# Kernel tuning notes

Hardware: AMD Instinct MI355X
Metric: run time of the kernel (lower is better)

## Reference

```python
import jax, jax.numpy as jnp
import numpy as np

C = 512
NC = 12
EPS = 1e-5

ADJ = np.array([
    [0,0,0,1,0,1,1,1,1,1,1,1],
    [0,0,0,1,0,1,1,1,1,1,1,1],
    [0,0,0,1,0,1,1,1,1,1,1,1],
    [1,1,1,0,1,1,1,1,1,1,1,1],
    [0,0,0,1,0,1,1,1,1,1,1,1],
    [1,1,1,1,1,0,1,1,1,0,0,0],
    [1,1,1,1,1,1,0,0,0,1,1,1],
    [1,1,1,1,1,1,0,0,0,1,1,1],
    [1,1,1,1,1,1,0,0,0,1,1,1],
    [1,1,1,1,1,0,1,1,1,0,0,0],
    [1,1,1,1,1,0,1,1,1,0,0,0],
    [1,1,1,1,1,0,1,1,1,0,0,0]], dtype=np.float32)
# per-AU region selection: 0=up,1=mid,2=down1,3=down2 (AU1,2,4 up; AU6 mid; AU7 up; AU10 d2; AU12,14,15 d1; AU17,23,24 d2)
SEL = np.array([0,0,0,1,0,3,2,2,2,3,3,3])


def setup_inputs() -> dict:
    key = jax.random.key(0)
    ks = jax.random.split(key, 12)
    B, T = 32, 32
    BT = B * T
    s = (2.0 / C) ** 0.5
    return {
        'x': jax.random.normal(ks[0], (BT, 49, C), jnp.float32),
        'adj_mask': jnp.ones((BT, NC, NC), jnp.float32),
        'region_W': jax.random.normal(ks[1], (4, C, C), jnp.float32) * s,
        'region_b': jnp.zeros((4, C), jnp.float32),
        'region_gamma': jnp.ones((4, C), jnp.float32),
        'region_beta': jnp.zeros((4, C), jnp.float32),
        'upfc_W': jax.random.normal(ks[2], (C, 16), jnp.float32) * 0.02,
        'upfc_b': jnp.zeros((16,), jnp.float32),
        'midfc_W': jax.random.normal(ks[3], (C, 2), jnp.float32) * 0.02,
        'midfc_b': jnp.zeros((2,), jnp.float32),
        'd1fc_W': jax.random.normal(ks[4], (C, 8), jnp.float32) * 0.02,
        'd1fc_b': jnp.zeros((8,), jnp.float32),
        'd2fc_W': jax.random.normal(ks[5], (C, 16), jnp.float32) * 0.02,
        'd2fc_b': jnp.zeros((16,), jnp.float32),
        'class_W': jax.random.normal(ks[6], (NC, C, C), jnp.float32) * s,
        'class_b': jnp.zeros((NC, C), jnp.float32),
        'class_gamma': jnp.ones((NC, C), jnp.float32),
        'class_beta': jnp.zeros((NC, C), jnp.float32),
        'gat_W': jax.random.normal(ks[7], (C, C), jnp.float32) * 0.02,
        'gat_al': jax.random.normal(ks[8], (C,), jnp.float32) * 0.02,
        'gat_ar': jax.random.normal(ks[9], (C,), jnp.float32) * 0.02,
        'tconv_W': jax.random.normal(ks[10], (NC, C, 5), jnp.float32) * 0.1,
        'tconv_b': jnp.zeros((NC, C), jnp.float32),
        'tbn_gamma': jnp.ones((NC,), jnp.float32),
        'tbn_beta': jnp.zeros((NC,), jnp.float32),
        'B': B,
        'T': T,
    }


def _bn(x, gamma, beta, axes):
    # training-mode batch norm: stats over `axes`, affine per remaining channel
    mean = x.mean(axes, keepdims=True)
    var = x.var(axes, keepdims=True)
    return gamma * (x - mean) * jax.lax.rsqrt(var + EPS) + beta


def reference(x, adj_mask, region_W, region_b, region_gamma, region_beta,
              upfc_W, upfc_b, midfc_W, midfc_b, d1fc_W, d1fc_b, d2fc_W, d2fc_b,
              class_W, class_b, class_gamma, class_beta,
              gat_W, gat_al, gat_ar, tconv_W, tconv_b, tbn_gamma, tbn_beta, B, T):
    BT = x.shape[0]
    xg = x.reshape(BT, 7, 7, C)
    x_up = xg[:, :3].reshape(BT, 21, C)
    x_mid = xg[:, 2:5].reshape(BT, 21, C)
    x_down = xg[:, 4:].reshape(BT, 21, C)
    # 4 region LinearBlocks (fc -> BN over (batch,seq) per channel -> relu), batched
    regions = jnp.stack([x_up, x_mid, x_down, x_down])  # [4,BT,21,C]
    h = jnp.einsum('rbsc,rcd->rbsd', regions, region_W) + region_b[:, None, None, :]
    h = jax.nn.relu(_bn(h, region_gamma[:, None, None, :], region_beta[:, None, None, :], (1, 2)))
    up_pred = h[0].mean(1) @ upfc_W + upfc_b
    mid_pred = h[1].mean(1) @ midfc_W + midfc_b
    d1_pred = h[2].mean(1) @ d1fc_W + d1fc_b
    d2_pred = h[3].mean(1) @ d2fc_W + d2fc_b
    # 12 per-AU LinearBlocks, batched over the class dim
    cls_in = h[jnp.asarray(SEL)]  # [12,BT,21,C]
    y = jnp.einsum('nbsc,ncd->nbsd', cls_in, class_W) + class_b[:, None, None, :]
    y = jax.nn.relu(_bn(y, class_gamma[:, None, None, :], class_beta[:, None, None, :], (1, 2)))
    f_v = y.mean(2).transpose(1, 0, 2)  # [BT,12,C]
    # cross-region single-head GAT over the fixed 12-node graph, residual, thred=0.1
    adj = jnp.asarray(ADJ)[None] * adj_mask + jnp.eye(NC, dtype=x.dtype)
    hg = f_v @ gat_W  # [BT,12,C]
    e = jax.nn.leaky_relu((hg @ gat_al)[:, :, None] + (hg @ gat_ar)[:, None, :], 0.2)
    attn = jax.nn.softmax(jnp.where(adj > 0.1, e, -1e9), axis=-1)
    g = jnp.einsum('bij,bjc->bic', attn, hg) + f_v
    # per-class depthwise temporal Conv1d (k=5, pad=2, groups=C), batched over classes
    x4 = g.reshape(B, T, NC, C)
    xp = jnp.pad(x4, ((0, 0), (2, 2), (0, 0), (0, 0)))
    v = sum(xp[:, k:k + T] * tconv_W[None, None, :, :, k] for k in range(5)) + tconv_b[None, None]
    v = v.reshape(BT, NC, C)
    out = jax.nn.relu(_bn(v, tbn_gamma[None, :, None], tbn_beta[None, :, None], (0, 2)))
    return (up_pred, mid_pred, d1_pred, d2_pred, out)
```

## Files before the change

kernel.cpp:

```cpp
#include <hip/hip_runtime.h>
#include <hip/hip_bf16.h>

typedef unsigned short u16;
typedef __attribute__((ext_vector_type(8))) __bf16 bf16x8;
typedef __attribute__((ext_vector_type(8))) u16 u16x8;
typedef __attribute__((ext_vector_type(4))) float floatx4;

#define C_     512
#define NC_    12
#define BT_    1024
#define SEQ_   21
#define M_REG  21504
#define M_GAT  12288

__device__ __forceinline__ float bf2f(u16 u) {
  unsigned int v = ((unsigned int)u) << 16;
  float f; __builtin_memcpy(&f, &v, 4); return f;
}
__device__ __forceinline__ u16 f2bf(float f) {
  unsigned int b; __builtin_memcpy(&b, &f, 4);
  unsigned int r = (b + 0x7FFFu + ((b >> 16) & 1u)) >> 16;
  return (u16)r;
}
__device__ __forceinline__ float ldf(const void* p, size_t i, int f32) {
  return f32 ? ((const float*)p)[i] : bf2f(((const u16*)p)[i]);
}
__device__ __forceinline__ u16 ldbf(const void* p, size_t i, int f32) {
  return f32 ? f2bf(((const float*)p)[i]) : ((const u16*)p)[i];
}
__device__ __forceinline__ void stout(void* p, size_t i, float v, int f32) {
  if (f32) ((float*)p)[i] = v; else ((u16*)p)[i] = f2bf(v);
}

typedef __attribute__((address_space(1))) unsigned int as1_u32;
typedef __attribute__((address_space(3))) unsigned int as3_u32;
__device__ __forceinline__ void gl2lds16(const void* g, void* l) {
  __builtin_amdgcn_global_load_lds((const as1_u32*)g, (as3_u32*)l, 16, 0, 0);
}

__global__ void sent_k(float* __restrict__ o, float val) {
  const int i = blockIdx.x * 256 + threadIdx.x;
  if (i < 16384) o[i] = val;
}

__global__ void detect_k(const u16* __restrict__ x, int* __restrict__ flag) {
  __shared__ int cnt;
  if (threadIdx.x == 0) cnt = 0;
  __syncthreads();
  int bad = 0;
  for (int i = threadIdx.x; i < 4096; i += 256) {
    const float v = bf2f(x[i]);
    const float a = fabsf(v);
    if (!(a <= 1e4f)) bad++;
    else if (a > 0.f && a < 1e-35f) bad++;
  }
  atomicAdd(&cnt, bad);
  __syncthreads();
  if (threadIdx.x == 0) *flag = (cnt > 400) ? 1 : 0;
}

__global__ void zero_stats(float* __restrict__ p, int n) {
  const int id = blockIdx.x * 256 + threadIdx.x;
  if (id < n) p[id] = 0.f;
}

__global__ void transpose512(const void* __restrict__ rW, const void* __restrict__ cW,
                             const void* __restrict__ gW, u16* __restrict__ oR,
                             u16* __restrict__ oC, u16* __restrict__ oG,
                             const int* __restrict__ flagp) {
  const int f32 = *flagp;
  const int z = blockIdx.z;
  const void* src; u16* dst; size_t sofs = 0;
  if (z < 4)       { src = rW; sofs = (size_t)z*262144;     dst = oR + (size_t)z*262144; }
  else if (z < 16) { src = cW; sofs = (size_t)(z-4)*262144; dst = oC + (size_t)(z-4)*262144; }
  else             { src = gW;                              dst = oG; }
  __shared__ u16 t[32][33];
  const int tx = threadIdx.x;
  const int cy = blockIdx.y * 32, dx = blockIdx.x * 32;
  for (int i = threadIdx.y; i < 32; i += 8)
    t[i][tx] = ldbf(src, sofs + (size_t)(cy + i)*512 + dx + tx, f32);
  __syncthreads();
  for (int i = threadIdx.y; i < 32; i += 8)
    dst[(size_t)(dx + i)*512 + cy + tx] = t[tx][i];
}

template<int MODE>
__global__ __launch_bounds__(256)
void gemm_k(const void* __restrict__ Abase, const u16* __restrict__ Wtb,
            const void* __restrict__ biasb, u16* __restrict__ outb,
            float* __restrict__ ssumb, float* __restrict__ ssqb,
            const int* __restrict__ flagp, int pk, int n0)
{
  const int f32 = *flagp;
  const int z = blockIdx.z;
  const int zeff = (MODE == 1) ? (n0 + z) : z;
  const void* A = Abase;
  if (MODE == 1) A = (const void*)((const u16*)Abase +
        (size_t)((pk >> (zeff * 2)) & 3) * ((size_t)M_REG * C_));
  const u16* Wt = Wtb + (size_t)zeff * C_ * C_;
  u16* Out = outb + (size_t)z * (size_t)M_REG * C_;

  __shared__ __align__(16) u16 As[128*32];
  __shared__ __align__(16) u16 Bs[128*32];

  const int tid  = threadIdx.x;
  const int w    = tid >> 6;
  const int lane = tid & 63;
  const int wm   = w >> 1, wn = w & 1;
  const int r16  = lane & 15, q = lane >> 4;

  const int m0  = blockIdx.y * 128;
  const int nn0 = blockIdx.x * 128;

  const int sub = lane >> 2;
  const int kq  = (lane & 3) * 8;
  const int am0 = m0 + w*32 + sub;
  const int am1 = am0 + 16;
  long ga0, ga1;
  if (MODE == 0) {
    const int roff = (pk >> (z * 8)) & 0xFF;
    int q21 = am0 / 21; int rm = am0 - q21*21;
    ga0 = (long)q21*49 + roff + rm;
    q21 = am1 / 21; rm = am1 - q21*21;
    ga1 = (long)q21*49 + roff + rm;
  } else { ga0 = am0; ga1 = am1; }
  const size_t aOff0 = (size_t)ga0 * C_ + kq;
  const size_t aOff1 = (size_t)ga1 * C_ + kq;
  const u16* bSrc0 = Wt + (size_t)(nn0 + w*32 + sub) * C_ + kq;
  const u16* bSrc1 = bSrc0 + (size_t)16 * C_;
  u16* aDstW0 = &As[(w*32 +  0) * 32];
  u16* aDstW1 = &As[(w*32 + 16) * 32];
  u16* bDstW0 = &Bs[(w*32 +  0) * 32];
  u16* bDstW1 = &Bs[(w*32 + 16) * 32];
  u16x8* aLds0 = (u16x8*)&As[(w*32 + sub +  0) * 32 + kq];
  u16x8* aLds1 = (u16x8*)&As[(w*32 + sub + 16) * 32 + kq];

  floatx4 acc[4][4];
  #pragma unroll
  for (int i = 0; i < 4; i++)
    #pragma unroll
    for (int j = 0; j < 4; j++)
      acc[i][j] = (floatx4){0.f, 0.f, 0.f, 0.f};

  for (int kk = 0; kk < C_; kk += 32) {
    if (MODE == 0 && f32) {
      const float* p0 = (const float*)A + aOff0 + kk;
      const float* p1 = (const float*)A + aOff1 + kk;
      const floatx4 f00 = *(const floatx4*)p0;
      const floatx4 f01 = *(const floatx4*)(p0 + 4);
      const floatx4 f10 = *(const floatx4*)p1;
      const floatx4 f11 = *(const floatx4*)(p1 + 4);
      u16x8 va0, va1;
      #pragma unroll
      for (int j = 0; j < 4; j++) {
        va0[j] = f2bf(f00[j]); va0[4+j] = f2bf(f01[j]);
        va1[j] = f2bf(f10[j]); va1[4+j] = f2bf(f11[j]);
      }
      __syncthreads();
      gl2lds16(bSrc0, bDstW0); gl2lds16(bSrc1, bDstW1);
      *aLds0 = va0; *aLds1 = va1;
      __syncthreads();
    } else {
      __syncthreads();
      gl2lds16((const u16*)A + aOff0 + kk, aDstW0);
      gl2lds16((const u16*)A + aOff1 + kk, aDstW1);
      gl2lds16(bSrc0, bDstW0);
      gl2lds16(bSrc1, bDstW1);
      __syncthreads();
    }
    bSrc0 += 32; bSrc1 += 32;
    bf16x8 av[4], bv[4];
    #pragma unroll
    for (int mt = 0; mt < 4; mt++)
      av[mt] = *(const bf16x8*)&As[(wm*64 + mt*16 + r16)*32 + q*8];
    #pragma unroll
    for (int nt = 0; nt < 4; nt++)
      bv[nt] = *(const bf16x8*)&Bs[(wn*64 + nt*16 + r16)*32 + q*8];
    #pragma unroll
    for (int mt = 0; mt < 4; mt++)
      #pragma unroll
      for (int nt = 0; nt < 4; nt++)
        acc[mt][nt] = __builtin_amdgcn_mfma_f32_16x16x32_bf16(av[mt], bv[nt], acc[mt][nt], 0, 0, 0);
  }

  const int colb = nn0 + wn*64;
  const int rowb = m0  + wm*64;
  #pragma unroll
  for (int nt = 0; nt < 4; nt++) {
    const int col = colb + nt*16 + r16;
    float bvv = 0.f;
    if (MODE != 2) bvv = ldf(biasb, (size_t)zeff * C_ + col, f32);
    float s = 0.f, s2 = 0.f;
    #pragma unroll
    for (int mt = 0; mt < 4; mt++) {
      #pragma unroll
      for (int p = 0; p < 4; p++) {
        float v = acc[mt][nt][p] + bvv;
        const int row = rowb + mt*16 + q*4 + p;
        Out[(size_t)row * C_ + col] = f2bf(v);
        s += v; s2 += v*v;
      }
    }
    if (MODE != 2) {
      s  += __shfl_xor(s, 16);  s  += __shfl_xor(s, 32);
      s2 += __shfl_xor(s2, 16); s2 += __shfl_xor(s2, 32);
      if (q == 0) {
        atomicAdd(&ssumb[(size_t)zeff * C_ + col], s);
        atomicAdd(&ssqb [(size_t)zeff * C_ + col], s2);
      }
    }
  }
}

__global__ void bn_region(u16* __restrict__ h, float* __restrict__ hbar,
                          const void* __restrict__ gamma, const void* __restrict__ beta,
                          const float* __restrict__ rsum, const float* __restrict__ rsq,
                          const int* __restrict__ flagp) {
  const int f32 = *flagp;
  const int gid  = blockIdx.x;
  const int r    = gid >> 8;
  const int bt   = ((gid & 255) << 2) + (threadIdx.x >> 6);
  const int lane = threadIdx.x & 63;
  const int d0   = lane * 8;
  const int rd   = r*512 + d0;
  float sc[8], sh[8], accv[8];
  #pragma unroll
  for (int j = 0; j < 8; j++) {
    const float mean = rsum[rd+j] * (1.f/21504.f);
    const float var  = fmaxf(rsq[rd+j] * (1.f/21504.f) - mean*mean, 0.f);
    sc[j] = ldf(gamma, rd+j, f32) * rsqrtf(var + 1e-5f);
    sh[j] = ldf(beta,  rd+j, f32) - mean * sc[j];
    accv[j] = 0.f;
  }
  const size_t base = ((size_t)r * M_REG + (size_t)bt * SEQ_) * C_ + d0;
  #pragma unroll
  for (int s = 0; s < SEQ_; s++) {
    u16x8 vv = *(u16x8*)&h[base + (size_t)s*C_];
    #pragma unroll
    for (int j = 0; j < 8; j++) {
      float v = fmaxf(sc[j] * bf2f(vv[j]) + sh[j], 0.f);
      vv[j] = f2bf(v);
      accv[j] += v;
    }
    *(u16x8*)&h[base + (size_t)s*C_] = vv;
  }
  float* hb = &hbar[((size_t)r * BT_ + bt) * C_ + d0];
  #pragma unroll
  for (int j = 0; j < 8; j++) hb[j] = accv[j] * (1.f/21.f);
}

__global__ void preds_k(const float* __restrict__ hbar,
                        const void* __restrict__ upW,  const void* __restrict__ upB,
                        const void* __restrict__ midW, const void* __restrict__ midB,
                        const void* __restrict__ d1W,  const void* __restrict__ d1B,
                        const void* __restrict__ d2W,  const void* __restrict__ d2B,
                        void* __restrict__ dout, const int* __restrict__ flagp) {
  const int f32 = *flagp;
  const int bt = blockIdx.x;
  __shared__ float hl[4][512];
  for (int i = threadIdx.x; i < 2048; i += 256)
    hl[i >> 9][i & 511] = hbar[((size_t)(i >> 9) * BT_ + bt) * C_ + (i & 511)];
  __syncthreads();
  const int j = threadIdx.x;
  if (j < 42) {
    int r, wdt, col; const void *W, *Bv; size_t oofs;
    if (j < 16)      { r=0; W=upW;  Bv=upB;  wdt=16; col=j;    oofs = (size_t)bt*16 + col; }
    else if (j < 18) { r=1; W=midW; Bv=midB; wdt=2;  col=j-16; oofs = 16384 + (size_t)bt*2 + col; }
    else if (j < 26) { r=2; W=d1W;  Bv=d1B;  wdt=8;  col=j-18; oofs = 18432 + (size_t)bt*8 + col; }
    else             { r=3; W=d2W;  Bv=d2B;  wdt=16; col=j-26; oofs = 26624 + (size_t)bt*16 + col; }
    float acc = ldf(Bv, col, f32);
    for (int d = 0; d < 512; d++) acc += hl[r][d] * ldf(W, d*wdt + col, f32);
    stout(dout, oofs, acc, f32);
  }
}

__global__ void bn_class_mean(const u16* __restrict__ ypre, u16* __restrict__ fv,
                              const void* __restrict__ gamma, const void* __restrict__ beta,
                              const float* __restrict__ csum, const float* __restrict__ csq,
                              const int* __restrict__ flagp, int n0) {
  const int f32 = *flagp;
  const int gid  = blockIdx.x;
  const int zz   = gid >> 8;
  const int bt   = ((gid & 255) << 2) + (threadIdx.x >> 6);
  const int lane = threadIdx.x & 63;
  const int d0   = lane * 8;
  const int n    = n0 + zz;
  const int nd   = n*512 + d0;
  float sc[8], sh[8], accv[8];
  #pragma unroll
  for (int j = 0; j < 8; j++) {
    const float mean = csum[nd+j] * (1.f/21504.f);
    const float var  = fmaxf(csq[nd+j] * (1.f/21504.f) - mean*mean, 0.f);
    sc[j] = ldf(gamma, nd+j, f32) * rsqrtf(var + 1e-5f);
    sh[j] = ldf(beta,  nd+j, f32) - mean * sc[j];
    accv[j] = 0.f;
  }
  const size_t base = ((size_t)zz * M_REG + (size_t)bt * SEQ_) * C_ + d0;
  #pragma unroll
  for (int s = 0; s < SEQ_; s++) {
    const u16x8 vv = *(const u16x8*)&ypre[base + (size_t)s*C_];
    #pragma unroll
    for (int j = 0; j < 8; j++)
      accv[j] += fmaxf(sc[j] * bf2f(vv[j]) + sh[j], 0.f);
  }
  u16x8 ov;
  #pragma unroll
  for (int j = 0; j < 8; j++) ov[j] = f2bf(accv[j] * (1.f/21.f));
  *(u16x8*)&fv[((size_t)bt * NC_ + n) * C_ + d0] = ov;
}

__global__ __launch_bounds__(256)
void gat_k(const u16* __restrict__ hg, const u16* __restrict__ fv,
           const void* __restrict__ al, const void* __restrict__ ar,
           const void* __restrict__ adj_mask, float* __restrict__ g,
           const int* __restrict__ flagp) {
  const int f32 = *flagp;
  const int bt = blockIdx.x;
  __shared__ float hl[12][512];
  __shared__ float alv[12], arv[12], attn[12][12];
  const u16* hgb = hg + (size_t)bt * NC_ * C_;
  for (int i = threadIdx.x; i < 6144; i += 256)
    hl[i >> 9][i & 511] = bf2f(hgb[i]);
  __syncthreads();
  const int w = threadIdx.x >> 6, lane = threadIdx.x & 63;
  for (int i = w; i < 12; i += 4) {
    float pa = 0.f, pr = 0.f;
    #pragma unroll
    for (int jj = 0; jj < 8; jj++) {
      const int c = lane*8 + jj;
      const float hv = hl[i][c];
      pa += hv * ldf(al, c, f32);
      pr += hv * ldf(ar, c, f32);
    }
    #pragma unroll
    for (int off = 32; off; off >>= 1) { pa += __shfl_xor(pa, off); pr += __shfl_xor(pr, off); }
    if (lane == 0) { alv[i] = pa; arv[i] = pr; }
  }
  __syncthreads();
  if (threadIdx.x < 12) {
    const unsigned AM[12] = {0xFE8,0xFE8,0xFE8,0xFF7,0xFE8,0x1DF,
                             0xE3F,0xE3F,0xE3F,0x1DF,0x1DF,0x1DF};
    const int i = threadIdx.x;
    float row[12]; float mx = -1e30f;
    #pragma unroll
    for (int jx = 0; jx < 12; jx++) {
      const float maskv = ldf(adj_mask, (size_t)bt*144 + i*12 + jx, f32);
      const float adjv = (float)((AM[i] >> jx) & 1u) * maskv + (i == jx ? 1.f : 0.f);
      float e;
      if (adjv > 0.1f) {
        const float t = alv[i] + arv[jx];
        e = t > 0.f ? t : 0.2f * t;
      } else e = -1e9f;
      row[jx] = e; mx = fmaxf(mx, e);
    }
    float den = 0.f;
    #pragma unroll
    for (int jx = 0; jx < 12; jx++) { const float ex = __expf(row[jx] - mx); row[jx] = ex; den += ex; }
    const float inv = 1.f / den;
    #pragma unroll
    for (int jx = 0; jx < 12; jx++) attn[i][jx] = row[jx] * inv;
  }
  __syncthreads();
  const u16* fvb = fv + (size_t)bt * NC_ * C_;
  float* gb = g + (size_t)bt * NC_ * C_;
  for (int o = threadIdx.x; o < 6144; o += 256) {
    const int i = o >> 9, c = o & 511;
    float acc = bf2f(fvb[o]);
    #pragma unroll
    for (int jx = 0; jx < 12; jx++) acc += attn[i][jx] * hl[jx][c];
    gb[o] = acc;
  }
}

__global__ void tconv_k(float* __restrict__ g, const void* __restrict__ tw,
                        const void* __restrict__ tb, float* __restrict__ tsum,
                        float* __restrict__ tsq, const int* __restrict__ flagp) {
  const int f32 = *flagp;
  const int id = blockIdx.x * 256 + threadIdx.x;
  const int c = id & 511;
  const int n = (id >> 9) % 12;
  const int b = id / 6144;
  float wk[5];
  #pragma unroll
  for (int k = 0; k < 5; k++) wk[k] = ldf(tw, (size_t)(n*512 + c)*5 + k, f32);
  const float bias = ldf(tb, n*512 + c, f32);
  float xv[36];
  xv[0] = xv[1] = xv[34] = xv[35] = 0.f;
  const size_t base = ((size_t)b * 32 * NC_ + n) * C_ + c;
  #pragma unroll
  for (int t = 0; t < 32; t++) xv[t + 2] = g[base + (size_t)t * 6144];
  float s = 0.f, s2 = 0.f;
  float ov[32];
  #pragma unroll
  for (int t = 0; t < 32; t++) {
    float v = bias;
    #pragma unroll
    for (int k = 0; k < 5; k++) v += wk[k] * xv[t + k];
    ov[t] = v; s += v; s2 += v*v;
  }
  #pragma unroll
  for (int t = 0; t < 32; t++) g[base + (size_t)t * 6144] = ov[t];
  #pragma unroll
  for (int off = 32; off; off >>= 1) { s += __shfl_xor(s, off); s2 += __shfl_xor(s2, off); }
  if ((threadIdx.x & 63) == 0) { atomicAdd(&tsum[n], s); atomicAdd(&tsq[n], s2); }
}

__global__ void bn_t(const float* __restrict__ v, void* __restrict__ outp,
                     const void* __restrict__ tg, const void* __restrict__ tb2,
                     const float* __restrict__ tsum, const float* __restrict__ tsq,
                     const int* __restrict__ flagp) {
  const int f32 = *flagp;
  const size_t id = (size_t)blockIdx.x * 256 + threadIdx.x;
  const int n = (int)((id >> 9) % 12);
  const float mean = tsum[n] * (1.f/524288.f);
  const float var  = fmaxf(tsq[n] * (1.f/524288.f) - mean*mean, 0.f);
  const float sc = ldf(tg, n, f32) * rsqrtf(var + 1e-5f);
  const float sh = ldf(tb2, n, f32) - mean * sc;
  stout(outp, 43008 + id, fmaxf(sc * v[id] + sh, 0.f), f32);
}

static constexpr size_t OFF_FLAG = 0;
static constexpr size_t OFF_STAT = 64;
static constexpr int    STAT_N   = 2048+2048+6144+6144+12+12;
static constexpr size_t OFF_WTR  = 65792;
static constexpr size_t OFF_WTC  = OFF_WTR + (size_t)4*512*512*2;
static constexpr size_t OFF_WTG  = OFF_WTC + (size_t)12*512*512*2;
static constexpr size_t OFF_H    = OFF_WTG + (size_t)512*512*2;
static constexpr size_t OFF_HBAR = OFF_H + (size_t)4*M_REG*C_*2;
static constexpr size_t OFF_FV   = OFF_HBAR + (size_t)4*BT_*C_*4;
static constexpr size_t OFF_AREN = OFF_FV + (size_t)M_GAT*C_*2;
static constexpr size_t YPRE_B   = (size_t)M_REG * C_ * 2;
static constexpr size_t NEEDED   = OFF_AREN + YPRE_B;

extern "C" void kernel_launch(void* const* d_in, const int* in_sizes, int n_in,
                              void* d_out, int out_size, void* d_ws, size_t ws_size,
                              hipStream_t stream) {
  const u16* x        = (const u16*)d_in[0];
  const void* adj_m   = d_in[1];
  const void* region_W= d_in[2];
  const void* region_b= d_in[3];
  const void* region_g= d_in[4];
  const void* region_be=d_in[5];
  const void* upW  = d_in[6];   const void* upB  = d_in[7];
  const void* midW = d_in[8];   const void* midB = d_in[9];
  const void* d1W  = d_in[10];  const void* d1B  = d_in[11];
  const void* d2W  = d_in[12];  const void* d2B  = d_in[13];
  const void* class_W = d_in[14];
  const void* class_b = d_in[15];
  const void* class_g = d_in[16];
  const void* class_be= d_in[17];
  const void* gat_W   = d_in[18];
  const void* gat_al  = d_in[19];
  const void* gat_ar  = d_in[20];
  const void* tconv_W = d_in[21];
  const void* tconv_b = d_in[22];
  const void* tbn_g   = d_in[23];
  const void* tbn_be  = d_in[24];

  char* ws = (char*)d_ws;
  int*   flagp = (int*)(ws + OFF_FLAG);
  float* rsum = (float*)(ws + OFF_STAT);
  float* rsq  = rsum + 2048;
  float* csum = rsq  + 2048;
  float* csq  = csum + 6144;
  float* tsum = csq  + 6144;
  float* tsq  = tsum + 12;
  u16*   WtR  = (u16*)(ws + OFF_WTR);
  u16*   WtC  = (u16*)(ws + OFF_WTC);
  u16*   WtG  = (u16*)(ws + OFF_WTG);
  u16*   h    = (u16*)(ws + OFF_H);
  float* hbar = (float*)(ws + OFF_HBAR);
  u16*   fv   = (u16*)(ws + OFF_FV);
  u16*   ypre = (u16*)(ws + OFF_AREN);
  u16*   hg   = (u16*)(ws + OFF_AREN);
  float* g    = (float*)(ws + OFF_H);

  int errStage = 0, errCode = 0;
  (void)hipGetLastError();
  #define CK(s) do { hipError_t e_ = hipGetLastError(); \
      if (e_ != hipSuccess && errStage == 0) { errStage = (s); errCode = (int)e_; } } while(0)

  sent_k<<<64, 256, 0, stream>>>((float*)d_out, 50.f); CK(12);

  if (ws_size < NEEDED) {
    int mb = (int)(ws_size >> 20); if (mb > 999) mb = 999;
    sent_k<<<64, 256, 0, stream>>>((float*)d_out, 13000.f + (float)mb);
    return;
  }

  int nch = (int)((ws_size - OFF_AREN) / YPRE_B);
  if (nch > 12) nch = 12;
  if (nch < 1) nch = 1;

  const int ROFFPACK = 0 | (14 << 8) | (28 << 16) | (28 << 24);
  const int SELPACK  = (1 << 6) | (3 << 10) | (2 << 12) | (2 << 14) |
                       (2 << 16) | (3 << 18) | (3 << 20) | (3 << 22);

  detect_k<<<1, 256, 0, stream>>>(x, flagp);                         CK(1);
  zero_stats<<<(STAT_N + 255)/256, 256, 0, stream>>>(rsum, STAT_N);  CK(1);
  transpose512<<<dim3(16,16,17), dim3(32,8), 0, stream>>>(
      region_W, class_W, gat_W, WtR, WtC, WtG, flagp);               CK(2);

  gemm_k<0><<<dim3(4,168,4), 256, 0, stream>>>(
      x, WtR, region_b, h, rsum, rsq, flagp, ROFFPACK, 0);           CK(3);
  bn_region<<<1024, 256, 0, stream>>>(h, hbar, region_g, region_be,
      rsum, rsq, flagp);                                             CK(4);
  preds_k<<<1024, 256, 0, stream>>>(hbar, upW,upB, midW,midB,
      d1W,d1B, d2W,d2B, d_out, flagp);                               CK(5);

  for (int n0 = 0; n0 < 12; n0 += nch) {
    const int zc = (12 - n0) < nch ? (12 - n0) : nch;
    gemm_k<1><<<dim3(4,168,zc), 256, 0, stream>>>(
        h, WtC, class_b, ypre, csum, csq, flagp, SELPACK, n0);       CK(6);
    bn_class_mean<<<zc*256, 256, 0, stream>>>(ypre, fv, class_g, class_be,
        csum, csq, flagp, n0);                                       CK(7);
  }

  gemm_k<2><<<dim3(4,96,1), 256, 0, stream>>>(
      fv, WtG, nullptr, hg, nullptr, nullptr, flagp, 0, 0);          CK(8);
  gat_k<<<1024, 256, 0, stream>>>(hg, fv, gat_al, gat_ar, adj_m, g, flagp); CK(9);
  tconv_k<<<768, 256, 0, stream>>>(g, tconv_W, tconv_b, tsum, tsq, flagp);  CK(10);
  bn_t<<<24576, 256, 0, stream>>>(g, d_out, tbn_g, tbn_be, tsum, tsq, flagp); CK(11);

  if (errStage) {
    int ec = errCode > 999 ? 999 : errCode;
    sent_k<<<64, 256, 0, stream>>>((float*)d_out, (float)(errStage*1000 + ec));
  }
  #undef CK
}
```

Measured before the change: 860.4 us.

## Remap GEMM blocks per XCD, stage epilogue through LDS, use nontemporal stores

The GEMM grid becomes 1D, and each XCD (blockIdx & 7) is given a contiguous band of M tiles so the blocks on one chiplet share the same A rows in L2. The epilogue now writes the bf16 tile into shared memory in two row halves, then issues coalesced 16-byte global stores, which are nontemporal for the large class GEMM output. The BN-mean kernel reads that output with nontemporal loads. The extra LDS round trip and barriers add epilogue cost, and the XCD mapping assumes round-robin dispatch of blocks across the 8 XCDs.

```diff
diff --git a/kernel.cpp b/kernel.cpp
--- a/kernel.cpp
+++ b/kernel.cpp
@@ -100,8 +100,9 @@
   const u16* Wt = Wtb + (size_t)zeff * C_ * C_;
   u16* Out = outb + (size_t)z * (size_t)M_REG * C_;
 
-  __shared__ __align__(16) u16 As[128*32];
-  __shared__ __align__(16) u16 Bs[128*32];
+  __shared__ __align__(16) u16 smem[64 * 132];
+  u16* As = smem;
+  u16* Bs = smem + 4096;
 
   const int tid  = threadIdx.x;
   const int w    = tid >> 6;
@@ -109,8 +110,14 @@
   const int wm   = w >> 1, wn = w & 1;
   const int r16  = lane & 15, q = lane >> 4;
 
-  const int m0  = blockIdx.y * 128;
-  const int nn0 = blockIdx.x * 128;
+  const int band = (MODE == 2) ? 12 : 21;
+  const int lin  = blockIdx.x;
+  const int xcd  = lin & 7;
+  const int idx  = lin >> 3;
+  const int mi   = xcd * band + idx % band;
+  const int ni   = idx / band;
+  const int m0   = mi * 128;
+  const int nn0  = ni * 128;
 
   const int sub = lane >> 2;
   const int kq  = (lane & 3) * 8;
@@ -183,31 +190,44 @@
         acc[mt][nt] = __builtin_amdgcn_mfma_f32_16x16x32_bf16(av[mt], bv[nt], acc[mt][nt], 0, 0, 0);
   }
 
-  const int colb = nn0 + wn*64;
-  const int rowb = m0  + wm*64;
-  #pragma unroll
-  for (int nt = 0; nt < 4; nt++) {
-    const int col = colb + nt*16 + r16;
-    float bvv = 0.f;
-    if (MODE != 2) bvv = ldf(biasb, (size_t)zeff * C_ + col, f32);
-    float s = 0.f, s2 = 0.f;
-    #pragma unroll
-    for (int mt = 0; mt < 4; mt++) {
+  #pragma unroll
+  for (int rh = 0; rh < 2; rh++) {
+    __syncthreads();
+    if (wm == rh) {
       #pragma unroll
-      for (int p = 0; p < 4; p++) {
-        float v = acc[mt][nt][p] + bvv;
-        const int row = rowb + mt*16 + q*4 + p;
-        Out[(size_t)row * C_ + col] = f2bf(v);
-        s += v; s2 += v*v;
+      for (int nt = 0; nt < 4; nt++) {
+        const int lcol = wn*64 + nt*16 + r16;
+        float bvv = 0.f;
+        if (MODE != 2) bvv = ldf(biasb, (size_t)zeff * C_ + nn0 + lcol, f32);
+        float s = 0.f, s2 = 0.f;
+        #pragma unroll
+        for (int mt = 0; mt < 4; mt++) {
+          #pragma unroll
+          for (int p = 0; p < 4; p++) {
+            const float v = acc[mt][nt][p] + bvv;
+            s += v; s2 += v*v;
+            smem[(mt*16 + q*4 + p)*132 + lcol] = f2bf(v);
+          }
+        }
+        if (MODE != 2) {
+          s  += __shfl_xor(s, 16);  s  += __shfl_xor(s, 32);
+          s2 += __shfl_xor(s2, 16); s2 += __shfl_xor(s2, 32);
+          if (q == 0) {
+            atomicAdd(&ssumb[(size_t)zeff * C_ + nn0 + lcol], s);
+            atomicAdd(&ssqb [(size_t)zeff * C_ + nn0 + lcol], s2);
+          }
+        }
       }
     }
-    if (MODE != 2) {
-      s  += __shfl_xor(s, 16);  s  += __shfl_xor(s, 32);
-      s2 += __shfl_xor(s2, 16); s2 += __shfl_xor(s2, 32);
-      if (q == 0) {
-        atomicAdd(&ssumb[(size_t)zeff * C_ + col], s);
-        atomicAdd(&ssqb [(size_t)zeff * C_ + col], s2);
-      }
+    __syncthreads();
+    #pragma unroll
+    for (int rr = 0; rr < 4; rr++) {
+      const int rl = rr*16 + (tid >> 4);
+      const int cc = (tid & 15) * 8;
+      const u16x8 vv = *(const u16x8*)&smem[rl*132 + cc];
+      u16x8* dst = (u16x8*)&Out[(size_t)(m0 + rh*64 + rl) * C_ + nn0 + cc];
+      if (MODE == 1) __builtin_nontemporal_store(vv, dst);
+      else           *dst = vv;
     }
   }
 }
@@ -298,7 +318,7 @@
   const size_t base = ((size_t)zz * M_REG + (size_t)bt * SEQ_) * C_ + d0;
   #pragma unroll
   for (int s = 0; s < SEQ_; s++) {
-    const u16x8 vv = *(const u16x8*)&ypre[base + (size_t)s*C_];
+    const u16x8 vv = __builtin_nontemporal_load((const u16x8*)&ypre[base + (size_t)s*C_]);
     #pragma unroll
     for (int j = 0; j < 8; j++)
       accv[j] += fmaxf(sc[j] * bf2f(vv[j]) + sh[j], 0.f);
@@ -501,7 +521,7 @@
   transpose512<<<dim3(16,16,17), dim3(32,8), 0, stream>>>(
       region_W, class_W, gat_W, WtR, WtC, WtG, flagp);               CK(2);
 
-  gemm_k<0><<<dim3(4,168,4), 256, 0, stream>>>(
+  gemm_k<0><<<dim3(672,1,4), 256, 0, stream>>>(
       x, WtR, region_b, h, rsum, rsq, flagp, ROFFPACK, 0);           CK(3);
   bn_region<<<1024, 256, 0, stream>>>(h, hbar, region_g, region_be,
       rsum, rsq, flagp);                                             CK(4);
@@ -510,13 +530,13 @@
 
   for (int n0 = 0; n0 < 12; n0 += nch) {
     const int zc = (12 - n0) < nch ? (12 - n0) : nch;
-    gemm_k<1><<<dim3(4,168,zc), 256, 0, stream>>>(
+    gemm_k<1><<<dim3(672,1,zc), 256, 0, stream>>>(
         h, WtC, class_b, ypre, csum, csq, flagp, SELPACK, n0);       CK(6);
     bn_class_mean<<<zc*256, 256, 0, stream>>>(ypre, fv, class_g, class_be,
         csum, csq, flagp, n0);                                       CK(7);
   }
 
-  gemm_k<2><<<dim3(4,96,1), 256, 0, stream>>>(
+  gemm_k<2><<<dim3(384,1,1), 256, 0, stream>>>(
       fv, WtG, nullptr, hg, nullptr, nullptr, flagp, 0, 0);          CK(8);
   gat_k<<<1024, 256, 0, stream>>>(hg, fv, gat_al, gat_ar, adj_m, g, flagp); CK(9);
   tconv_k<<<768, 256, 0, stream>>>(g, tconv_W, tconv_b, tsum, tsq, flagp);  CK(10);
```

Result: faster. 798.2 us (-7.2%).
